# Optimization experiments

Measured on AMD Instinct MI355X. Metric: run time of the kernel, lower is better.

Reference implementation:

```python
import jax, jax.numpy as jnp
import numpy as np

D_MODEL = 1024
N_HEADS = 16
D_HEAD = 64
GROUP_SIZE = 2
N_GROUPS = N_HEADS // GROUP_SIZE


def setup_inputs() -> dict:
    key = jax.random.key(0)
    k1, k2, k3, k4, k5 = jax.random.split(key, 5)
    def xavier(k, shape):
        fan_in, fan_out = shape[0], int(np.prod(shape[1:]))
        bound = float(np.sqrt(6.0 / (fan_in + fan_out)))
        return jax.random.uniform(k, shape, jnp.float32, -bound, bound)
    return {
        'resid': jax.random.normal(k1, (2, 2048, D_MODEL), jnp.float32),
        'W_Q': xavier(k2, (D_MODEL, N_HEADS, D_HEAD)),
        'W_K': xavier(k3, (D_MODEL, N_GROUPS, D_HEAD)),
        'W_V': xavier(k4, (D_MODEL, N_GROUPS, D_HEAD)),
        'W_out': xavier(k5, (D_HEAD, N_HEADS, D_MODEL)),
        'b_out': jnp.zeros((D_MODEL,), jnp.float32),
    }


def reference(resid, W_Q, W_K, W_V, W_out, b_out):
    batch, seq, _ = resid.shape
    # q: [b, s, n_heads, d_head] -> [b, s, n_groups, group_size, d_head]
    q = jnp.einsum('bsd,dhe->bshe', resid, W_Q)
    q = q.reshape(batch, seq, N_GROUPS, GROUP_SIZE, D_HEAD)
    k = jnp.einsum('bsd,dge->bsge', resid, W_K)  # [b, s, g, e]
    v = jnp.einsum('bsd,dge->bsge', resid, W_V)
    # scores: [b, g, group_size, qseq, kseq]
    scores = jnp.einsum('bqgre,bkge->bgrqk', q, k) / jnp.sqrt(jnp.float32(D_HEAD))
    causal_mask = jnp.triu(jnp.ones((seq, seq), bool), k=1)
    scores = jnp.where(causal_mask, jnp.float32(-1000000.0), scores)
    probs = jax.nn.softmax(scores, axis=-1)
    # z: [b, q, g, r, e]
    z = jnp.einsum('bgrqk,bkge->bqgre', probs, v)
    z = z.reshape(batch, seq, N_HEADS, D_HEAD)
    out = jnp.einsum('bshe,ehd->bsd', z, W_out) + b_out
    return out
```

## Files before the change

### kernel.cpp

```cpp
#include <hip/hip_runtime.h>

#define BATCH   2
#define SEQ     2048
#define DMODEL  1024
#define NHEADS  16
#define DHEAD   64
#define NGROUPS 8
#define NTOK    (BATCH * SEQ)
#define QKV_N   2048

typedef unsigned short ushort_t;
typedef unsigned int u32;
typedef __attribute__((ext_vector_type(8))) short short8;
typedef __attribute__((ext_vector_type(4))) float f32x4;

#define MFMA16(a, b, c) __builtin_amdgcn_mfma_f32_16x16x32_bf16((a), (b), (c), 0, 0, 0)

#define GLOAD16(gp, lp)                                                        \
    __builtin_amdgcn_global_load_lds(                                          \
        (const u32 __attribute__((address_space(1)))*)(gp),                    \
        (u32 __attribute__((address_space(3)))*)(lp), 16, 0, 0)

__device__ __forceinline__ ushort_t f2bu(float x) {
    unsigned u = __builtin_bit_cast(unsigned, x);
    unsigned r = (u + 0x7fffu + ((u >> 16) & 1u)) >> 16;
    return (ushort_t)r;
}

__global__ __launch_bounds__(256) void prep(
    const float* __restrict__ resid,
    const float* __restrict__ Wq, const float* __restrict__ Wk,
    const float* __restrict__ Wv, const float* __restrict__ Wout,
    ushort_t* __restrict__ rbf, ushort_t* __restrict__ Wt,
    ushort_t* __restrict__ Wot)
{
    __shared__ float Ws[64][65];
    const int t = threadIdx.x;
    const int bid = blockIdx.x;

    if (bid < 4096) {
        const int i4 = bid * 256 + t;
        union { float4 v; float f[4]; } a;
        a.v = *reinterpret_cast<const float4*>(resid + (size_t)i4 * 4);
        union { uint2 v; ushort_t u[4]; } o;
        #pragma unroll
        for (int j = 0; j < 4; ++j) o.u[j] = f2bu(a.f[j]);
        *reinterpret_cast<uint2*>(rbf + (size_t)i4 * 4) = o.v;
        return;
    }

    if (bid < 4096 + 512) {
        const int rel = bid - 4096;
        const int k0 = (rel & 15) * 64;
        const int n0 = (rel >> 4) * 64;

        const float* src; int stride, boff;
        if (n0 < 1024)       { src = Wq; stride = 1024; boff = n0; }
        else if (n0 < 1536)  { src = Wk; stride = 512;  boff = n0 - 1024; }
        else                 { src = Wv; stride = 512;  boff = n0 - 1536; }

        #pragma unroll
        for (int i = 0; i < 4; ++i) {
            const int c = i * 256 + t;
            const int row = c >> 4, cc = (c & 15) * 4;
            union { float4 v; float f[4]; } a;
            a.v = *reinterpret_cast<const float4*>(
                src + (size_t)(k0 + row) * stride + boff + cc);
            #pragma unroll
            for (int j = 0; j < 4; ++j) Ws[row][cc + j] = a.f[j];
        }
        __syncthreads();
        #pragma unroll
        for (int i = 0; i < 2; ++i) {
            const int c = i * 256 + t;
            const int nr = c >> 3, kc = (c & 7) * 8;
            union { uint4 v; ushort_t u[8]; } o;
            #pragma unroll
            for (int j = 0; j < 8; ++j) o.u[j] = f2bu(Ws[kc + j][nr]);
            *reinterpret_cast<uint4*>(Wt + (size_t)(n0 + nr) * 1024 + k0 + kc) = o.v;
        }
        return;
    }

    {
        const int rel = bid - 4608;
        const int d0 = (rel & 15) * 64;
        const int h  = rel >> 4;

        #pragma unroll
        for (int i = 0; i < 4; ++i) {
            const int c = i * 256 + t;
            const int e = c >> 4, dd = (c & 15) * 4;
            union { float4 v; float f[4]; } a;
            a.v = *reinterpret_cast<const float4*>(
                Wout + (size_t)(e * 16 + h) * 1024 + d0 + dd);
            #pragma unroll
            for (int j = 0; j < 4; ++j) Ws[e][dd + j] = a.f[j];
        }
        __syncthreads();
        #pragma unroll
        for (int i = 0; i < 2; ++i) {
            const int c = i * 256 + t;
            const int dr = c >> 3, ec = (c & 7) * 8;
            union { uint4 v; ushort_t u[8]; } o;
            #pragma unroll
            for (int j = 0; j < 8; ++j) o.u[j] = f2bu(Ws[ec + j][dr]);
            *reinterpret_cast<uint4*>(Wot + (size_t)(d0 + dr) * 1024 + h * 64 + ec) = o.v;
        }
    }
}

__global__ __launch_bounds__(256) void tr_v(
    const ushort_t* __restrict__ qkv, ushort_t* __restrict__ Vt)
{
    __shared__ ushort_t T[64][72];
    const int t  = threadIdx.x;
    const int s0 = blockIdx.x * 64;
    const int g  = blockIdx.y;
    const int b  = blockIdx.z;

    #pragma unroll
    for (int i = 0; i < 2; ++i) {
        const int c = i * 256 + t;
        const int row = c >> 3, ec = (c & 7) * 8;
        *reinterpret_cast<uint4*>(&T[row][ec]) =
            *reinterpret_cast<const uint4*>(
                qkv + (size_t)(b * SEQ + s0 + row) * QKV_N + 1536 + g * 64 + ec);
    }
    __syncthreads();
    #pragma unroll
    for (int i = 0; i < 2; ++i) {
        const int c = i * 256 + t;
        const int er = c >> 3, sc = (c & 7) * 8;
        union { uint4 v; ushort_t u[8]; } o;
        #pragma unroll
        for (int j = 0; j < 8; ++j) o.u[j] = T[sc + j][er];
        *reinterpret_cast<uint4*>(
            Vt + (size_t)((b * NGROUPS + g) * 64 + er) * SEQ + s0 + sc) = o.v;
    }
}

__global__ __launch_bounds__(512) void qkv_gemm(
    const ushort_t* __restrict__ A, const ushort_t* __restrict__ Bt,
    ushort_t* __restrict__ C)
{
    __shared__ ushort_t As[128][64];
    __shared__ ushort_t Bs[128][64];

    const int t = threadIdx.x;
    const int wave = t >> 6, lane = t & 63;
    const int quad = lane >> 4, x = lane & 15;
    const int wm = (wave >> 1) * 32, wn = (wave & 1) * 64;
    const int m0 = blockIdx.y * 128, n0 = blockIdx.x * 128;

    const int sr8 = lane >> 3;
    const int gc  = (lane & 7) ^ sr8;

    f32x4 acc[2][4];
    #pragma unroll
    for (int i = 0; i < 2; ++i)
        #pragma unroll
        for (int j = 0; j < 4; ++j) acc[i][j] = (f32x4)(0.f);

    for (int k0 = 0; k0 < 1024; k0 += 64) {
        #pragma unroll
        for (int s = 0; s < 2; ++s) {
            const int r0 = (wave * 2 + s) * 8;
            GLOAD16(A  + (size_t)(m0 + r0 + sr8) * 1024 + k0 + gc * 8, &As[r0][0]);
            GLOAD16(Bt + (size_t)(n0 + r0 + sr8) * 1024 + k0 + gc * 8, &Bs[r0][0]);
        }
        __syncthreads();
        #pragma unroll
        for (int j = 0; j < 2; ++j) {
            const int cs = ((j * 4 + quad) ^ (x & 7)) * 8;
            short8 af[2], bf[4];
            #pragma unroll
            for (int mt = 0; mt < 2; ++mt)
                af[mt] = *reinterpret_cast<const short8*>(&As[wm + mt * 16 + x][cs]);
            #pragma unroll
            for (int nt = 0; nt < 4; ++nt)
                bf[nt] = *reinterpret_cast<const short8*>(&Bs[wn + nt * 16 + x][cs]);
            #pragma unroll
            for (int mt = 0; mt < 2; ++mt)
                #pragma unroll
                for (int nt = 0; nt < 4; ++nt)
                    acc[mt][nt] = MFMA16(af[mt], bf[nt], acc[mt][nt]);
        }
        __syncthreads();
    }

    #pragma unroll
    for (int mt = 0; mt < 2; ++mt)
        #pragma unroll
        for (int nt = 0; nt < 4; ++nt)
            #pragma unroll
            for (int r = 0; r < 4; ++r) {
                const int row = m0 + wm + mt * 16 + quad * 4 + r;
                const int col = n0 + wn + nt * 16 + x;
                C[(size_t)row * QKV_N + col] = f2bu(acc[mt][nt][r]);
            }
}

__global__ __launch_bounds__(512) void out_gemm(
    const ushort_t* __restrict__ A, const ushort_t* __restrict__ Bt,
    const float* __restrict__ bias, float* __restrict__ C)
{
    __shared__ ushort_t As[128][64];
    __shared__ ushort_t Bs[64][64];

    const int t = threadIdx.x;
    const int wave = t >> 6, lane = t & 63;
    const int quad = lane >> 4, x = lane & 15;
    const int wm = (wave >> 1) * 32, wn = (wave & 1) * 32;
    const int m0 = blockIdx.y * 128, n0 = blockIdx.x * 64;

    const int sr8 = lane >> 3;
    const int gc  = (lane & 7) ^ sr8;

    f32x4 acc[2][2];
    #pragma unroll
    for (int i = 0; i < 2; ++i)
        #pragma unroll
        for (int j = 0; j < 2; ++j) acc[i][j] = (f32x4)(0.f);

    for (int k0 = 0; k0 < 1024; k0 += 64) {
        #pragma unroll
        for (int s = 0; s < 2; ++s) {
            const int r0 = (wave * 2 + s) * 8;
            GLOAD16(A + (size_t)(m0 + r0 + sr8) * 1024 + k0 + gc * 8, &As[r0][0]);
        }
        {
            const int r0 = wave * 8;
            GLOAD16(Bt + (size_t)(n0 + r0 + sr8) * 1024 + k0 + gc * 8, &Bs[r0][0]);
        }
        __syncthreads();
        #pragma unroll
        for (int j = 0; j < 2; ++j) {
            const int cs = ((j * 4 + quad) ^ (x & 7)) * 8;
            short8 af[2], bf[2];
            #pragma unroll
            for (int mt = 0; mt < 2; ++mt)
                af[mt] = *reinterpret_cast<const short8*>(&As[wm + mt * 16 + x][cs]);
            #pragma unroll
            for (int nt = 0; nt < 2; ++nt)
                bf[nt] = *reinterpret_cast<const short8*>(&Bs[wn + nt * 16 + x][cs]);
            #pragma unroll
            for (int mt = 0; mt < 2; ++mt)
                #pragma unroll
                for (int nt = 0; nt < 2; ++nt)
                    acc[mt][nt] = MFMA16(af[mt], bf[nt], acc[mt][nt]);
        }
        __syncthreads();
    }

    float bv[2];
    #pragma unroll
    for (int nt = 0; nt < 2; ++nt) bv[nt] = bias[n0 + wn + nt * 16 + x];

    #pragma unroll
    for (int mt = 0; mt < 2; ++mt)
        #pragma unroll
        for (int nt = 0; nt < 2; ++nt)
            #pragma unroll
            for (int r = 0; r < 4; ++r) {
                const int row = m0 + wm + mt * 16 + quad * 4 + r;
                const int col = n0 + wn + nt * 16 + x;
                C[(size_t)row * 1024 + col] = acc[mt][nt][r] + bv[nt];
            }
}

__global__ __launch_bounds__(512, 4) void attn(
    const ushort_t* __restrict__ qkv, const ushort_t* __restrict__ Vt,
    ushort_t* __restrict__ z)
{
    __shared__ ushort_t smem[5 * 64 * 64];
    ushort_t (*KsB)[64][64]  = (ushort_t(*)[64][64])(smem);
    ushort_t (*VtsB)[64][64] = (ushort_t(*)[64][64])(smem + 2 * 64 * 64);
    ushort_t (*Ps)[64]       = (ushort_t(*)[64])(smem + 4 * 64 * 64);
    float* Ob = (float*)smem;
    float* Lb = (float*)(smem + 4 * 64 * 64);

    const int t = threadIdx.x;
    const int wave = t >> 6, lane = t & 63;
    const int quad = lane >> 4, x = lane & 15;
    const int rw = wave & 3;
    const int kw = wave >> 2;

    const int h  = blockIdx.x;
    const int qp = blockIdx.y;
    const int b  = blockIdx.z;
    const int g  = h >> 1;

    const int srow = t >> 3;
    const int schk = (t & 7) ^ (srow & 7);
    const int sec  = (t & 7) * 8;

    const ushort_t* kbase = qkv + (size_t)(b * SEQ) * QKV_N + 1024 + g * DHEAD + sec;
    const ushort_t* vbase = Vt + (size_t)((b * NGROUPS + g) * 64 + srow) * SEQ + sec;

    short8 ones;
    #pragma unroll
    for (int i = 0; i < 8; ++i) ones[i] = (short)0x3F80;

    #pragma unroll
    for (int phase = 0; phase < 2; ++phase) {
        const int qt = phase ? (31 - qp) : qp;
        const int qrow0 = qt * 64;

        short8 aq[2];
        {
            const size_t qr = (size_t)(b * SEQ + qrow0 + rw * 16 + x);
            #pragma unroll
            for (int ks = 0; ks < 2; ++ks)
                aq[ks] = *reinterpret_cast<const short8*>(
                    qkv + qr * QKV_N + h * DHEAD + ks * 32 + quad * 8);
        }

        f32x4 o[4];
        #pragma unroll
        for (int nt = 0; nt < 4; ++nt) o[nt] = (f32x4)(0.f);
        f32x4 lacc = (f32x4)(0.f);

        {
            uint4 kr = *reinterpret_cast<const uint4*>(kbase + (size_t)srow * QKV_N);
            uint4 vr = *reinterpret_cast<const uint4*>(vbase);
            *reinterpret_cast<uint4*>(&KsB[0][srow][schk * 8])  = kr;
            *reinterpret_cast<uint4*>(&VtsB[0][srow][schk * 8]) = vr;
        }
        __syncthreads();

        for (int kt = 0; kt <= qt; ++kt) {
            const int cur = kt & 1;

            uint4 kr, vr;
            if (kt < qt) {
                kr = *reinterpret_cast<const uint4*>(
                    kbase + (size_t)((kt + 1) * 64 + srow) * QKV_N);
                vr = *reinterpret_cast<const uint4*>(vbase + (kt + 1) * 64);
            }

            const bool diag  = (kt == qt);
            const bool wlive = !diag || (kw * 32 <= rw * 16 + 15);

            if (wlive) {
                f32x4 s[2];
                __builtin_amdgcn_s_setprio(1);
                #pragma unroll
                for (int nt = 0; nt < 2; ++nt) {
                    const bool live = !diag || (kw * 32 + nt * 16 <= rw * 16 + 15);
                    if (live) {
                        s[nt] = (f32x4)(0.f);
                        #pragma unroll
                        for (int ks = 0; ks < 2; ++ks) {
                            const int cs = ((ks * 4 + quad) ^ (x & 7)) * 8;
                            short8 bk = *reinterpret_cast<const short8*>(
                                &KsB[cur][kw * 32 + nt * 16 + x][cs]);
                            s[nt] = MFMA16(aq[ks], bk, s[nt]);
                        }
                    }
                }
                __builtin_amdgcn_s_setprio(0);

                #pragma unroll
                for (int r = 0; r < 4; ++r) {
                    const int prow = rw * 16 + quad * 4 + r;
                    const int pswz = (prow & 7) << 3;
                    #pragma unroll
                    for (int nt = 0; nt < 2; ++nt) {
                        const bool live = !diag || (kw * 32 + nt * 16 <= rw * 16 + 15);
                        float p = 0.f;
                        if (live) {
                            const bool masked = diag &&
                                (kw * 32 + nt * 16 + x > rw * 16 + quad * 4 + r);
                            p = masked ? 0.f : __expf(s[nt][r] * 0.125f);
                        }
                        Ps[prow][(kw * 32 + nt * 16 + x) ^ pswz] = f2bu(p);
                    }
                }

                __builtin_amdgcn_s_setprio(1);
                {
                    const int cap = ((kw * 4 + quad) ^ (x & 7)) * 8;
                    short8 ap = *reinterpret_cast<const short8*>(
                        &Ps[rw * 16 + x][cap]);
                    #pragma unroll
                    for (int nt = 0; nt < 4; ++nt) {
                        short8 bv = *reinterpret_cast<const short8*>(
                            &VtsB[cur][nt * 16 + x][cap]);
                        o[nt] = MFMA16(ap, bv, o[nt]);
                    }
                    lacc = MFMA16(ap, ones, lacc);
                }
                __builtin_amdgcn_s_setprio(0);
            }

            if (kt < qt) {
                *reinterpret_cast<uint4*>(&KsB[cur ^ 1][srow][schk * 8])  = kr;
                *reinterpret_cast<uint4*>(&VtsB[cur ^ 1][srow][schk * 8]) = vr;
            }
            __syncthreads();
        }

        if (kw == 1) {
            #pragma unroll
            for (int nt = 0; nt < 4; ++nt)
                #pragma unroll
                for (int r = 0; r < 4; ++r)
                    Ob[(rw * 16 + quad * 4 + r) * 64 + nt * 16 + x] = o[nt][r];
            #pragma unroll
            for (int r = 0; r < 4; ++r)
                Lb[(rw * 16 + quad * 4 + r) * 16 + x] = lacc[r];
        }
        __syncthreads();
        if (kw == 0) {
            #pragma unroll
            for (int nt = 0; nt < 4; ++nt)
                #pragma unroll
                for (int r = 0; r < 4; ++r)
                    o[nt][r] += Ob[(rw * 16 + quad * 4 + r) * 64 + nt * 16 + x];
            float inv[4];
            #pragma unroll
            for (int r = 0; r < 4; ++r)
                inv[r] = 1.f / (lacc[r] + Lb[(rw * 16 + quad * 4 + r) * 16 + x]);
            #pragma unroll
            for (int nt = 0; nt < 4; ++nt)
                #pragma unroll
                for (int r = 0; r < 4; ++r) {
                    const int row = qrow0 + rw * 16 + quad * 4 + r;
                    z[(size_t)(b * SEQ + row) * 1024 + h * DHEAD + nt * 16 + x] =
                        f2bu(o[nt][r] * inv[r]);
                }
        }
        __syncthreads();
    }
}

extern "C" void kernel_launch(void* const* d_in, const int* in_sizes, int n_in,
                              void* d_out, int out_size, void* d_ws, size_t ws_size,
                              hipStream_t stream)
{
    const float* resid = (const float*)d_in[0];
    const float* Wq    = (const float*)d_in[1];
    const float* Wk    = (const float*)d_in[2];
    const float* Wv    = (const float*)d_in[3];
    const float* Wout  = (const float*)d_in[4];
    const float* bout  = (const float*)d_in[5];
    float* out = (float*)d_out;

    ushort_t* rbf   = (ushort_t*)d_ws;
    ushort_t* wqkvt = rbf   + (size_t)NTOK * DMODEL;
    ushort_t* woutt = wqkvt + (size_t)QKV_N * DMODEL;
    ushort_t* qkv   = woutt + (size_t)DMODEL * DMODEL;
    ushort_t* z     = qkv   + (size_t)NTOK * QKV_N;
    ushort_t* vt    = rbf;

    prep     <<<dim3(4864), 256, 0, stream>>>(resid, Wq, Wk, Wv, Wout,
                                              rbf, wqkvt, woutt);
    qkv_gemm <<<dim3(16, 32), 512, 0, stream>>>(rbf, wqkvt, qkv);
    tr_v     <<<dim3(SEQ / 64, NGROUPS, BATCH), 256, 0, stream>>>(qkv, vt);
    attn     <<<dim3(16, 16, 2), 512, 0, stream>>>(qkv, vt, z);
    out_gemm <<<dim3(16, 32), 512, 0, stream>>>(z, woutt, bout, out);
}
```

Before: 162.0 us.

## Rewrite attention inner loop with 32x32 MFMA, register-resident P and 128-key tiles

The attention kernel now uses 32x32x16 bf16 MFMA with a transposed S^T = K·Q^T formulation, so probabilities stay in registers. They are packed with v_cvt_pk_bf16_f32 and rearranged with v_permlane32_swap instead of round-tripping through LDS. Key tiles grow to 128 keys split across 4 key-waves, with a tree reduction of partial outputs. Row sums are accumulated in scalar registers instead of an extra MFMA against ones, and z is written as vectorized 16-byte stores. This cuts LDS traffic and MFMA instruction count per tile, at the cost of a more complex multi-stage reduction and coarser causal masking granularity.

New measurement: 164.2 us, median of 2. Within noise of the previous version (+1.3%).

```diff
diff --git a/kernel.cpp b/kernel.cpp
--- a/kernel.cpp
+++ b/kernel.cpp
@@ -13,13 +13,21 @@
 typedef unsigned int u32;
 typedef __attribute__((ext_vector_type(8))) short short8;
 typedef __attribute__((ext_vector_type(4))) float f32x4;
+typedef __attribute__((ext_vector_type(16))) float f32x16;
 
 #define MFMA16(a, b, c) __builtin_amdgcn_mfma_f32_16x16x32_bf16((a), (b), (c), 0, 0, 0)
+#define MFMA32(a, b, c) __builtin_amdgcn_mfma_f32_32x32x16_bf16((a), (b), (c), 0, 0, 0)
 
 #define GLOAD16(gp, lp)                                                        \
     __builtin_amdgcn_global_load_lds(                                          \
         (const u32 __attribute__((address_space(1)))*)(gp),                    \
         (u32 __attribute__((address_space(3)))*)(lp), 16, 0, 0)
+
+#define CVTPK(dst, lo, hi) \
+    asm("v_cvt_pk_bf16_f32 %0, %1, %2" : "=v"(dst) : "v"(lo), "v"(hi))
+
+#define PLSWAP(a, b) \
+    asm("v_permlane32_swap_b32 %0, %1" : "+v"(a), "+v"(b))
 
 __device__ __forceinline__ ushort_t f2bu(float x) {
     unsigned u = __builtin_bit_cast(unsigned, x);
@@ -273,165 +281,216 @@
     const ushort_t* __restrict__ qkv, const ushort_t* __restrict__ Vt,
     ushort_t* __restrict__ z)
 {
-    __shared__ ushort_t smem[5 * 64 * 64];
-    ushort_t (*KsB)[64][64]  = (ushort_t(*)[64][64])(smem);
-    ushort_t (*VtsB)[64][64] = (ushort_t(*)[64][64])(smem + 2 * 64 * 64);
-    ushort_t (*Ps)[64]       = (ushort_t(*)[64])(smem + 4 * 64 * 64);
-    float* Ob = (float*)smem;
-    float* Lb = (float*)(smem + 4 * 64 * 64);
+    __shared__ ushort_t smem[4 * 128 * 64];
+    ushort_t (*Ks)[128][64]  = (ushort_t(*)[128][64])(smem);
+    ushort_t (*Vts)[64][128] = (ushort_t(*)[64][128])(smem + 2 * 128 * 64);
+    float* Ob1  = (float*)smem;
+    float* Ob3  = (float*)(smem + 128 * 64);
+    float* Ofin = (float*)(smem + 2 * 128 * 64);
+    float* Lb1  = (float*)(smem + 3 * 128 * 64);
+    float* Lb3  = Lb1 + 64;
 
     const int t = threadIdx.x;
     const int wave = t >> 6, lane = t & 63;
-    const int quad = lane >> 4, x = lane & 15;
-    const int rw = wave & 3;
-    const int kw = wave >> 2;
+    const int x31 = lane & 31, hi = lane >> 5;
+    const int rw = wave & 1;
+    const int kw = wave >> 1;
 
     const int h  = blockIdx.x;
     const int qp = blockIdx.y;
     const int b  = blockIdx.z;
     const int g  = h >> 1;
 
-    const int srow = t >> 3;
-    const int schk = (t & 7) ^ (srow & 7);
-    const int sec  = (t & 7) * 8;
-
-    const ushort_t* kbase = qkv + (size_t)(b * SEQ) * QKV_N + 1024 + g * DHEAD + sec;
-    const ushort_t* vbase = Vt + (size_t)((b * NGROUPS + g) * 64 + srow) * SEQ + sec;
-
-    short8 ones;
-    #pragma unroll
-    for (int i = 0; i < 8; ++i) ones[i] = (short)0x3F80;
+    const int krow = t >> 3;
+    const int kc   = t & 7;
+    const int vrow = t >> 4;
+    const int vc   = t & 15;
+
+    const ushort_t* kgb = qkv + (size_t)(b * SEQ) * QKV_N + 1024 + g * 64 + kc * 8;
+    const ushort_t* vgb = Vt + (size_t)((b * NGROUPS + g) * 64) * SEQ + vc * 8;
+
+    const int kswz = (kc ^ (krow & 7)) * 8;
+    const int vswz = (vc ^ (vrow & 15)) * 8;
+
+    const int qloc = rw * 32 + x31;
 
     #pragma unroll
     for (int phase = 0; phase < 2; ++phase) {
         const int qt = phase ? (31 - qp) : qp;
         const int qrow0 = qt * 64;
-
-        short8 aq[2];
+        const int nkt = (qt >> 1) + 1;
+
+        short8 aq[4];
+        #pragma unroll
+        for (int sl = 0; sl < 4; ++sl)
+            aq[sl] = *reinterpret_cast<const short8*>(
+                qkv + (size_t)(b * SEQ + qrow0 + qloc) * QKV_N + h * 64 + sl * 16 + hi * 8);
+
+        f32x16 o0 = (f32x16)(0.f), o1 = (f32x16)(0.f);
+        float lown = 0.f;
+
+        __syncthreads();
+
         {
-            const size_t qr = (size_t)(b * SEQ + qrow0 + rw * 16 + x);
-            #pragma unroll
-            for (int ks = 0; ks < 2; ++ks)
-                aq[ks] = *reinterpret_cast<const short8*>(
-                    qkv + qr * QKV_N + h * DHEAD + ks * 32 + quad * 8);
-        }
-
-        f32x4 o[4];
-        #pragma unroll
-        for (int nt = 0; nt < 4; ++nt) o[nt] = (f32x4)(0.f);
-        f32x4 lacc = (f32x4)(0.f);
-
-        {
-            uint4 kr = *reinterpret_cast<const uint4*>(kbase + (size_t)srow * QKV_N);
-            uint4 vr = *reinterpret_cast<const uint4*>(vbase);
-            *reinterpret_cast<uint4*>(&KsB[0][srow][schk * 8])  = kr;
-            *reinterpret_cast<uint4*>(&VtsB[0][srow][schk * 8]) = vr;
-        }
-        __syncthreads();
-
-        for (int kt = 0; kt <= qt; ++kt) {
+            uint4 a0 = *reinterpret_cast<const uint4*>(kgb + (size_t)krow * QKV_N);
+            uint4 a1 = *reinterpret_cast<const uint4*>(kgb + (size_t)(krow + 64) * QKV_N);
+            uint4 b0 = *reinterpret_cast<const uint4*>(vgb + (size_t)vrow * SEQ);
+            uint4 b1 = *reinterpret_cast<const uint4*>(vgb + (size_t)(vrow + 32) * SEQ);
+            *reinterpret_cast<uint4*>(&Ks[0][krow][kswz])       = a0;
+            *reinterpret_cast<uint4*>(&Ks[0][krow + 64][kswz])  = a1;
+            *reinterpret_cast<uint4*>(&Vts[0][vrow][vswz])      = b0;
+            *reinterpret_cast<uint4*>(&Vts[0][vrow + 32][vswz]) = b1;
+        }
+        __syncthreads();
+
+        for (int kt = 0; kt < nkt; ++kt) {
             const int cur = kt & 1;
-
-            uint4 kr, vr;
-            if (kt < qt) {
-                kr = *reinterpret_cast<const uint4*>(
-                    kbase + (size_t)((kt + 1) * 64 + srow) * QKV_N);
-                vr = *reinterpret_cast<const uint4*>(vbase + (kt + 1) * 64);
-            }
-
-            const bool diag  = (kt == qt);
-            const bool wlive = !diag || (kw * 32 <= rw * 16 + 15);
-
-            if (wlive) {
-                f32x4 s[2];
+            const bool more = (kt + 1 < nkt);
+
+            uint4 a0, a1, b0, b1;
+            if (more) {
+                const size_t kb = (size_t)((kt + 1) * 128);
+                a0 = *reinterpret_cast<const uint4*>(kgb + (kb + krow) * QKV_N);
+                a1 = *reinterpret_cast<const uint4*>(kgb + (kb + krow + 64) * QKV_N);
+                b0 = *reinterpret_cast<const uint4*>(vgb + (size_t)vrow * SEQ + kb);
+                b1 = *reinterpret_cast<const uint4*>(vgb + (size_t)(vrow + 32) * SEQ + kb);
+            }
+
+            const int cbase = kt * 128 + kw * 32;
+            const int qmin  = qrow0 + rw * 32;
+
+            if (cbase <= qmin + 31) {
+                const bool full = (cbase + 31 <= qmin);
+
+                f32x16 st = (f32x16)(0.f);
                 __builtin_amdgcn_s_setprio(1);
                 #pragma unroll
-                for (int nt = 0; nt < 2; ++nt) {
-                    const bool live = !diag || (kw * 32 + nt * 16 <= rw * 16 + 15);
-                    if (live) {
-                        s[nt] = (f32x4)(0.f);
-                        #pragma unroll
-                        for (int ks = 0; ks < 2; ++ks) {
-                            const int cs = ((ks * 4 + quad) ^ (x & 7)) * 8;
-                            short8 bk = *reinterpret_cast<const short8*>(
-                                &KsB[cur][kw * 32 + nt * 16 + x][cs]);
-                            s[nt] = MFMA16(aq[ks], bk, s[nt]);
-                        }
-                    }
+                for (int sl = 0; sl < 4; ++sl) {
+                    short8 ak = *reinterpret_cast<const short8*>(
+                        &Ks[cur][kw * 32 + x31][((sl * 2 + hi) ^ (x31 & 7)) * 8]);
+                    st = MFMA32(ak, aq[sl], st);
                 }
                 __builtin_amdgcn_s_setprio(0);
 
+                const int ql = qmin + x31 - cbase;
+                float p[16];
+                float s16 = 0.f;
                 #pragma unroll
-                for (int r = 0; r < 4; ++r) {
-                    const int prow = rw * 16 + quad * 4 + r;
-                    const int pswz = (prow & 7) << 3;
-                    #pragma unroll
-                    for (int nt = 0; nt < 2; ++nt) {
-                        const bool live = !diag || (kw * 32 + nt * 16 <= rw * 16 + 15);
-                        float p = 0.f;
-                        if (live) {
-                            const bool masked = diag &&
-                                (kw * 32 + nt * 16 + x > rw * 16 + quad * 4 + r);
-                            p = masked ? 0.f : __expf(s[nt][r] * 0.125f);
-                        }
-                        Ps[prow][(kw * 32 + nt * 16 + x) ^ pswz] = f2bu(p);
-                    }
+                for (int r = 0; r < 16; ++r) {
+                    const int keyoff = (r & 3) + 8 * (r >> 2);
+                    float pv = __expf(st[r] * 0.125f);
+                    if (!full) pv = (keyoff + 4 * hi > ql) ? 0.f : pv;
+                    p[r] = pv;
+                    s16 += pv;
                 }
+                lown += s16;
+
+                u32 pk0, pk1, pk2, pk3, pk4, pk5, pk6, pk7;
+                CVTPK(pk0, p[0],  p[1]);  CVTPK(pk1, p[2],  p[3]);
+                CVTPK(pk2, p[4],  p[5]);  CVTPK(pk3, p[6],  p[7]);
+                CVTPK(pk4, p[8],  p[9]);  CVTPK(pk5, p[10], p[11]);
+                CVTPK(pk6, p[12], p[13]); CVTPK(pk7, p[14], p[15]);
+                PLSWAP(pk0, pk2); PLSWAP(pk1, pk3);
+                PLSWAP(pk4, pk6); PLSWAP(pk5, pk7);
+                union { u32 u[4]; short8 s; } f0, f1;
+                f0.u[0] = pk0; f0.u[1] = pk1; f0.u[2] = pk2; f0.u[3] = pk3;
+                f1.u[0] = pk4; f1.u[1] = pk5; f1.u[2] = pk6; f1.u[3] = pk7;
 
                 __builtin_amdgcn_s_setprio(1);
-                {
-                    const int cap = ((kw * 4 + quad) ^ (x & 7)) * 8;
-                    short8 ap = *reinterpret_cast<const short8*>(
-                        &Ps[rw * 16 + x][cap]);
-                    #pragma unroll
-                    for (int nt = 0; nt < 4; ++nt) {
-                        short8 bv = *reinterpret_cast<const short8*>(
-                            &VtsB[cur][nt * 16 + x][cap]);
-                        o[nt] = MFMA16(ap, bv, o[nt]);
-                    }
-                    lacc = MFMA16(ap, ones, lacc);
+                #pragma unroll
+                for (int ks = 0; ks < 2; ++ks) {
+                    const short8 pf = ks ? f1.s : f0.s;
+                    short8 av0 = *reinterpret_cast<const short8*>(
+                        &Vts[cur][x31][((kw * 4 + ks * 2 + hi) ^ (x31 & 15)) * 8]);
+                    o0 = MFMA32(av0, pf, o0);
+                    short8 av1 = *reinterpret_cast<const short8*>(
+                        &Vts[cur][32 + x31][((kw * 4 + ks * 2 + hi) ^ (x31 & 15)) * 8]);
+                    o1 = MFMA32(av1, pf, o1);
                 }
                 __builtin_amdgcn_s_setprio(0);
             }
 
-            if (kt < qt) {
-                *reinterpret_cast<uint4*>(&KsB[cur ^ 1][srow][schk * 8])  = kr;
-                *reinterpret_cast<uint4*>(&VtsB[cur ^ 1][srow][schk * 8]) = vr;
+            if (more) {
+                *reinterpret_cast<uint4*>(&Ks[cur ^ 1][krow][kswz])       = a0;
+                *reinterpret_cast<uint4*>(&Ks[cur ^ 1][krow + 64][kswz])  = a1;
+                *reinterpret_cast<uint4*>(&Vts[cur ^ 1][vrow][vswz])      = b0;
+                *reinterpret_cast<uint4*>(&Vts[cur ^ 1][vrow + 32][vswz]) = b1;
             }
             __syncthreads();
         }
 
-        if (kw == 1) {
-            #pragma unroll
-            for (int nt = 0; nt < 4; ++nt)
-                #pragma unroll
-                for (int r = 0; r < 4; ++r)
-                    Ob[(rw * 16 + quad * 4 + r) * 64 + nt * 16 + x] = o[nt][r];
-            #pragma unroll
-            for (int r = 0; r < 4; ++r)
-                Lb[(rw * 16 + quad * 4 + r) * 16 + x] = lacc[r];
+        float ltot;
+        {
+            u32 la = __builtin_bit_cast(u32, lown), lb = la;
+            PLSWAP(la, lb);
+            const float lpart = __builtin_bit_cast(float, hi ? la : lb);
+            ltot = lown + lpart;
+        }
+
+        if (kw == 1 || kw == 3) {
+            float* Obx = (kw == 1) ? Ob1 : Ob3;
+            float* Lbx = (kw == 1) ? Lb1 : Lb3;
+            #pragma unroll
+            for (int r = 0; r < 16; ++r) {
+                const int e = (r & 3) + 8 * (r >> 2) + 4 * hi;
+                Obx[e * 64 + qloc]        = o0[r];
+                Obx[(32 + e) * 64 + qloc] = o1[r];
+            }
+            if (hi == 0) Lbx[qloc] = ltot;
+        }
+        __syncthreads();
+        if (kw == 0 || kw == 2) {
+            const float* Obx = (kw == 0) ? Ob1 : Ob3;
+            const float* Lbx = (kw == 0) ? Lb1 : Lb3;
+            #pragma unroll
+            for (int r = 0; r < 16; ++r) {
+                const int e = (r & 3) + 8 * (r >> 2) + 4 * hi;
+                o0[r] += Obx[e * 64 + qloc];
+                o1[r] += Obx[(32 + e) * 64 + qloc];
+            }
+            ltot += Lbx[qloc];
+        }
+        __syncthreads();
+        if (kw == 2) {
+            #pragma unroll
+            for (int r = 0; r < 16; ++r) {
+                const int e = (r & 3) + 8 * (r >> 2) + 4 * hi;
+                Ob1[e * 64 + qloc]        = o0[r];
+                Ob1[(32 + e) * 64 + qloc] = o1[r];
+            }
+            if (hi == 0) Lb1[qloc] = ltot;
         }
         __syncthreads();
         if (kw == 0) {
             #pragma unroll
-            for (int nt = 0; nt < 4; ++nt)
-                #pragma unroll
-                for (int r = 0; r < 4; ++r)
-                    o[nt][r] += Ob[(rw * 16 + quad * 4 + r) * 64 + nt * 16 + x];
-            float inv[4];
-            #pragma unroll
-            for (int r = 0; r < 4; ++r)
-                inv[r] = 1.f / (lacc[r] + Lb[(rw * 16 + quad * 4 + r) * 16 + x]);
-            #pragma unroll
-            for (int nt = 0; nt < 4; ++nt)
-                #pragma unroll
-                for (int r = 0; r < 4; ++r) {
-                    const int row = qrow0 + rw * 16 + quad * 4 + r;
-                    z[(size_t)(b * SEQ + row) * 1024 + h * DHEAD + nt * 16 + x] =
-                        f2bu(o[nt][r] * inv[r]);
-                }
-        }
-        __syncthreads();
+            for (int r = 0; r < 16; ++r) {
+                const int e = (r & 3) + 8 * (r >> 2) + 4 * hi;
+                o0[r] += Ob1[e * 64 + qloc];
+                o1[r] += Ob1[(32 + e) * 64 + qloc];
+            }
+            ltot += Lb1[qloc];
+            const float inv = 1.f / ltot;
+            #pragma unroll
+            for (int r = 0; r < 16; ++r) {
+                const int e = (r & 3) + 8 * (r >> 2) + 4 * hi;
+                Ofin[e * 64 + qloc]        = o0[r] * inv;
+                Ofin[(32 + e) * 64 + qloc] = o1[r] * inv;
+            }
+        }
+        __syncthreads();
+
+        {
+            const int q = t >> 3, ec = t & 7;
+            union { u32 u[4]; uint4 v; } pkz;
+            #pragma unroll
+            for (int j2 = 0; j2 < 4; ++j2) {
+                float v0 = Ofin[(ec * 8 + 2 * j2) * 64 + q];
+                float v1 = Ofin[(ec * 8 + 2 * j2 + 1) * 64 + q];
+                CVTPK(pkz.u[j2], v0, v1);
+            }
+            *reinterpret_cast<uint4*>(
+                z + (size_t)(b * SEQ + qrow0 + q) * 1024 + h * 64 + ec * 8) = pkz.v;
+        }
     }
 }
 
```
